# Optimization experiments

Measured on AMD Instinct MI355X. Metric: run time of the kernel, lower is better.

## Reference

```python
import jax, jax.numpy as jnp
import numpy as np

DIM = 1024
HEADS = 16
DIM_HEAD = 64
B = 4
N = 2048
INNER = HEADS * DIM_HEAD
SCALE = DIM_HEAD ** -0.5
NEG = -1e9


def setup_inputs() -> dict:
    key = jax.random.key(0)
    k1, k2, k3 = jax.random.split(key, 3)
    x = jax.random.normal(k1, (B, N, DIM), dtype=jnp.float32)
    w_qkv = jax.random.normal(k2, (DIM, 3 * INNER), dtype=jnp.float32) * (DIM ** -0.5)
    w_out = jax.random.normal(k3, (INNER, DIM), dtype=jnp.float32) * (INNER ** -0.5)
    b_out = jnp.zeros((DIM,), dtype=jnp.float32)
    return {"x": x, "w_qkv": w_qkv, "w_out": w_out, "b_out": b_out}


def reference(x, w_qkv, w_out, b_out):
    b, n, _ = x.shape
    qkv = x @ w_qkv  # [b, n, 3*inner]
    q, k, v = jnp.split(qkv, 3, axis=-1)
    # [b, n, inner] -> [b, h, n, d]
    split_heads = lambda t: t.reshape(b, n, HEADS, DIM_HEAD).transpose(0, 2, 1, 3)
    q, k, v = split_heads(q), split_heads(k), split_heads(v)
    dots = jnp.einsum('bhid,bhjd->bhij', q, k) * SCALE
    causal = jnp.tril(jnp.ones((n, n), dtype=bool))  # mask[i,j]=1 for j<=i
    dots = jnp.where(causal, dots, NEG)
    attn = jax.nn.softmax(dots, axis=-1)
    out = jnp.einsum('bhij,bhjd->bhid', attn, v)
    out = out.transpose(0, 2, 1, 3).reshape(b, n, INNER)
    return out @ w_out + b_out
```

## Files before the change

kernel.cpp:

```cpp
#include <hip/hip_runtime.h>

typedef unsigned short u16;
typedef unsigned int u32;
typedef __attribute__((ext_vector_type(8))) short short8;
typedef __attribute__((ext_vector_type(4))) float f32x4;
typedef __attribute__((ext_vector_type(4))) short short4v;
typedef __attribute__((ext_vector_type(2))) unsigned int uint2v;

#define MFMA_BF16(a, b, c) __builtin_amdgcn_mfma_f32_16x16x32_bf16((a), (b), (c), 0, 0, 0)

__device__ __forceinline__ void gl2lds16(const u16* g, u16* l) {
  __builtin_amdgcn_global_load_lds(
      (const __attribute__((address_space(1))) unsigned int*)g,
      (__attribute__((address_space(3))) unsigned int*)l, 16, 0, 0);
}

__device__ __forceinline__ u16 f2bf(float f) {
  union { float f; unsigned u; } v; v.f = f;
  unsigned r = v.u + 0x7fffu + ((v.u >> 16) & 1u);
  return (u16)(r >> 16);
}

__global__ void fill_one_f32(float* p, int n) {
  int i = blockIdx.x * blockDim.x + threadIdx.x;
  if (i < n) p[i] = 1.0f;
}

__global__ void prep_k(const float* __restrict__ x, u16* __restrict__ Xb,
                       const float* __restrict__ w_qkv, u16* __restrict__ wqkvT,
                       const float* __restrict__ w_out, u16* __restrict__ woutT) {
  __shared__ float tile[32][33];
  const int bid = blockIdx.x, t = threadIdx.x;
  if (bid < 2048) {
    const int base = (bid * 256 + t) * 16;
#pragma unroll
    for (int h = 0; h < 2; ++h) {
      const f32x4 v0 = *(const f32x4*)&x[base + h * 8];
      const f32x4 v1 = *(const f32x4*)&x[base + h * 8 + 4];
      short8 o;
      o[0] = (short)f2bf(v0.x); o[1] = (short)f2bf(v0.y);
      o[2] = (short)f2bf(v0.z); o[3] = (short)f2bf(v0.w);
      o[4] = (short)f2bf(v1.x); o[5] = (short)f2bf(v1.y);
      o[6] = (short)f2bf(v1.z); o[7] = (short)f2bf(v1.w);
      *(short8*)&Xb[base + h * 8] = o;
    }
    return;
  }
  const float* src; u16* dst; int R, C, bx, by;
  if (bid < 5120) {
    const int tb = bid - 2048;
    src = w_qkv; dst = wqkvT; R = 1024; C = 3072; bx = tb % 96; by = tb / 96;
  } else {
    const int tb = bid - 5120;
    src = w_out; dst = woutT; R = 1024; C = 1024; bx = tb % 32; by = tb / 32;
  }
  const int tx = t & 31, ty = t >> 5;
  const int r0 = by * 32, c0 = bx * 32;
#pragma unroll
  for (int i = 0; i < 4; ++i)
    tile[ty + i * 8][tx] = src[(size_t)(r0 + ty + i * 8) * C + c0 + tx];
  __syncthreads();
#pragma unroll
  for (int i = 0; i < 4; ++i)
    dst[(size_t)(c0 + ty + i * 8) * R + r0 + tx] = f2bf(tile[tx][ty + i * 8]);
}

template <int MODE>
__launch_bounds__(256, 2)
__global__ void gemm_bt_k(const u16* __restrict__ A, const u16* __restrict__ Bt,
                          int K, int Ncols,
                          u16* __restrict__ O0, u16* __restrict__ O1,
                          u16* __restrict__ O2,
                          float* __restrict__ Of, const float* __restrict__ biasf) {
  __shared__ __align__(16) u16 Alds[128 * 32];
  __shared__ __align__(16) u16 Blds[128 * 32];
  const int t = threadIdx.x;
  const int w = t >> 6, l = t & 63;
  const int quad = l >> 4, l16 = l & 15;
  const int m0 = blockIdx.y * 128, n0 = blockIdx.x * 128;
  const int wm = w & 1, wn = w >> 1;

  f32x4 acc[4][4];
#pragma unroll
  for (int a = 0; a < 4; ++a)
#pragma unroll
    for (int b = 0; b < 4; ++b) acc[a][b] = (f32x4){0.f, 0.f, 0.f, 0.f};

  const int c0 = w * 128 + l;

#pragma unroll 1
  for (int k0 = 0; k0 < K; k0 += 32) {
    {
      int c = c0;
      gl2lds16(A + (size_t)(m0 + (c >> 2)) * K + k0 + (c & 3) * 8,
               (u16*)((char*)Alds + c * 16));
      gl2lds16(Bt + (size_t)(n0 + (c >> 2)) * K + k0 + (c & 3) * 8,
               (u16*)((char*)Blds + c * 16));
      c = c0 + 64;
      gl2lds16(A + (size_t)(m0 + (c >> 2)) * K + k0 + (c & 3) * 8,
               (u16*)((char*)Alds + c * 16));
      gl2lds16(Bt + (size_t)(n0 + (c >> 2)) * K + k0 + (c & 3) * 8,
               (u16*)((char*)Blds + c * 16));
    }
    __syncthreads();
    short8 av[4], bv[4];
#pragma unroll
    for (int a = 0; a < 4; ++a)
      av[a] = *(const short8*)&Alds[(wm * 64 + a * 16 + l16) * 32 + quad * 8];
#pragma unroll
    for (int b = 0; b < 4; ++b)
      bv[b] = *(const short8*)&Blds[(wn * 64 + b * 16 + l16) * 32 + quad * 8];
#pragma unroll
    for (int a = 0; a < 4; ++a)
#pragma unroll
      for (int b = 0; b < 4; ++b)
        acc[a][b] = MFMA_BF16(av[a], bv[b], acc[a][b]);
    __syncthreads();
  }

#pragma unroll
  for (int a = 0; a < 4; ++a)
#pragma unroll
    for (int b = 0; b < 4; ++b) {
      const int row0 = m0 + wm * 64 + a * 16 + quad * 4;
      const int col = n0 + wn * 64 + b * 16 + l16;
      if (MODE == 0) {
        const int bb = row0 >> 11, n = row0 & 2047;
        const int which = col >> 10, j = col & 1023, h = j >> 6, d = j & 63;
        if (which == 2) {
          short4v o;
#pragma unroll
          for (int r = 0; r < 4; ++r) o[r] = (short)f2bf(acc[a][b][r]);
          *(short4v*)&O2[(((size_t)bb * 16 + h) * 64 + d) * 2048 + n] = o;
        } else {
          u16* dst = which ? O1 : O0;
#pragma unroll
          for (int r = 0; r < 4; ++r)
            dst[(((size_t)bb * 16 + h) * 2048 + (n + r)) * 64 + d] =
                f2bf(acc[a][b][r]);
        }
      } else {
#pragma unroll
        for (int r = 0; r < 4; ++r)
          Of[(size_t)(row0 + r) * Ncols + col] = acc[a][b][r] + biasf[col];
      }
    }
}

#define KSV 72
#define PS 72
__launch_bounds__(512, 2)
__global__ void flash_k8(const u16* __restrict__ Q, const u16* __restrict__ K,
                         const u16* __restrict__ VT, u16* __restrict__ AO) {
  __shared__ __align__(16) u16 Klds[2][64 * KSV];
  __shared__ __align__(16) u16 Vt[2][64 * KSV];
  __shared__ __align__(16) u16 Plds[8][16 * PS];
  const int t = threadIdx.x, w = t >> 6, l = t & 63;
  const int quad = l >> 4, l16 = l & 15;
  const int flat = blockIdx.x;
  const int bh = flat & 63;
  const int grp = flat >> 6;
  const int qi = (grp < 4) ? grp : (11 - grp);
  const size_t base = (size_t)bh * 2048 * 64;
  const u16* Qp = Q + base;
  const u16* Kp = K + base;
  const u16* VTp = VT + base;
  const int bb = bh >> 4, hh = bh & 15;
  const float SC = 0.125f;
  const float FM = 3.0f;

  const int kcp = t >> 3, kcd = (t & 7) * 8;
  const int vcd = t >> 3, vcp = (t & 7) * 8;

  short8 ones;
#pragma unroll
  for (int j = 0; j < 8; ++j) ones[j] = (short)0x3F80;

  const int qbase = qi * 256;

  short8 qf[2][2];
#pragma unroll
  for (int mi = 0; mi < 2; ++mi) {
    const int qrow = qbase + w * 32 + mi * 16 + l16;
    qf[mi][0] = *(const short8*)&Qp[(size_t)qrow * 64 + quad * 8];
    qf[mi][1] = *(const short8*)&Qp[(size_t)qrow * 64 + 32 + quad * 8];
  }

  f32x4 oacc[2][4], lacc[2];
#pragma unroll
  for (int mi = 0; mi < 2; ++mi) {
    lacc[mi] = (f32x4){0.f, 0.f, 0.f, 0.f};
#pragma unroll
    for (int df = 0; df < 4; ++df) oacc[mi][df] = (f32x4){0.f, 0.f, 0.f, 0.f};
  }

  const int nkt = 4 * qi + 4;
  const int wlo = qbase + w * 32;
  const int whi = wlo + 31;

  short8 kv = *(const short8*)&Kp[(size_t)kcp * 64 + kcd];
  short8 vv = *(const short8*)&VTp[(size_t)vcd * 2048 + vcp];

#pragma unroll 1
  for (int kt = 0; kt < nkt; ++kt) {
    const int buf = kt & 1;
    *(short8*)&Klds[buf][kcp * KSV + kcd] = kv;
    *(short8*)&Vt[buf][vcd * KSV + vcp] = vv;
    __syncthreads();

    if (kt + 1 < nkt) {
      kv = *(const short8*)&Kp[(size_t)((kt + 1) * 64 + kcp) * 64 + kcd];
      vv = *(const short8*)&VTp[(size_t)vcd * 2048 + (kt + 1) * 64 + vcp];
    }

    const bool skip = (kt * 64 > whi);
    if (!skip) {
      f32x4 sa[2][4];
#pragma unroll
      for (int nf = 0; nf < 4; ++nf) {
        const short8 kf0 = *(const short8*)&Klds[buf][(nf * 16 + l16) * KSV + quad * 8];
        const short8 kf1 = *(const short8*)&Klds[buf][(nf * 16 + l16) * KSV + 32 + quad * 8];
#pragma unroll
        for (int mi = 0; mi < 2; ++mi) {
          f32x4 s = (f32x4){0.f, 0.f, 0.f, 0.f};
          s = MFMA_BF16(kf0, qf[mi][0], s);
          s = MFMA_BF16(kf1, qf[mi][1], s);
          sa[mi][nf] = s;
        }
      }

      const bool needmask = (kt * 64 + 63 > wlo);
      short8 pf[2][2];
#pragma unroll
      for (int mi = 0; mi < 2; ++mi) {
        const int qrow = qbase + w * 32 + mi * 16 + l16;
#pragma unroll
        for (int nf = 0; nf < 4; ++nf) {
          u32 dw[2];
#pragma unroll
          for (int h = 0; h < 2; ++h) {
            u32 pk = 0;
#pragma unroll
            for (int r2 = 0; r2 < 2; ++r2) {
              const int r = h * 2 + r2;
              float arg = fmaf(sa[mi][nf][r], SC, -FM);
              if (needmask) {
                const int kp = kt * 64 + nf * 16 + quad * 4 + r;
                arg = (kp <= qrow) ? arg : -1e9f;
              }
              union { float f; unsigned u; } pu;
              pu.f = __expf(arg);
              pk |= (u32)((pu.u + 0x8000u) >> 16) << (16 * r2);
            }
            dw[h] = pk;
          }
          *(uint2v*)&Plds[w][l16 * PS + nf * 16 + quad * 4] = (uint2v){dw[0], dw[1]};
        }
        pf[mi][0] = *(const short8*)&Plds[w][l16 * PS + quad * 8];
        pf[mi][1] = *(const short8*)&Plds[w][l16 * PS + 32 + quad * 8];
        lacc[mi] = MFMA_BF16(pf[mi][0], ones, lacc[mi]);
        lacc[mi] = MFMA_BF16(pf[mi][1], ones, lacc[mi]);
      }

#pragma unroll
      for (int df = 0; df < 4; ++df) {
        const int rowb = (df * 16 + l16) * KSV;
        const short8 vf0 = *(const short8*)&Vt[buf][rowb + quad * 8];
        const short8 vf1 = *(const short8*)&Vt[buf][rowb + 32 + quad * 8];
#pragma unroll
        for (int mi = 0; mi < 2; ++mi) {
          oacc[mi][df] = MFMA_BF16(pf[mi][0], vf0, oacc[mi][df]);
          oacc[mi][df] = MFMA_BF16(pf[mi][1], vf1, oacc[mi][df]);
        }
      }
    }
  }

#pragma unroll
  for (int mi = 0; mi < 2; ++mi) {
    const int srow = qbase + w * 32 + mi * 16 + quad * 4;
#pragma unroll
    for (int df = 0; df < 4; ++df)
#pragma unroll
      for (int r = 0; r < 4; ++r) {
        const int n = srow + r;
        const int d = df * 16 + l16;
        AO[((size_t)bb * 2048 + n) * 1024 + hh * 64 + d] =
            f2bf(oacc[mi][df][r] / lacc[mi][r]);
      }
  }
}

extern "C" void kernel_launch(void* const* d_in, const int* in_sizes, int n_in,
                              void* d_out, int out_size, void* d_ws, size_t ws_size,
                              hipStream_t stream) {
  const float* x = (const float*)d_in[0];
  const float* w_qkv = (const float*)d_in[1];
  const float* w_out = (const float*)d_in[2];
  const float* b_out = (const float*)d_in[3];
  float* out = (float*)d_out;

  const size_t MB = 1024 * 1024;
  if (ws_size < 72 * MB) {
    fill_one_f32<<<(out_size + 255) / 256, 256, 0, stream>>>(out, out_size);
    return;
  }

  char* ws = (char*)d_ws;
  u16* wqkvT = (u16*)(ws);
  u16* woutT = (u16*)(ws + 6 * MB);
  u16* Xb = (u16*)(ws + 8 * MB);
  u16* AO = Xb;
  u16* Qb = (u16*)(ws + 24 * MB);
  u16* Kb = (u16*)(ws + 40 * MB);
  u16* VbT = (u16*)(ws + 56 * MB);

  prep_k<<<6144, 256, 0, stream>>>(x, Xb, w_qkv, wqkvT, w_out, woutT);
  gemm_bt_k<0><<<dim3(3072 / 128, 8192 / 128), 256, 0, stream>>>(
      Xb, wqkvT, 1024, 3072, Qb, Kb, VbT, nullptr, nullptr);
  flash_k8<<<512, 512, 0, stream>>>(Qb, Kb, VbT, AO);
  gemm_bt_k<1><<<dim3(1024 / 128, 8192 / 128), 256, 0, stream>>>(
      AO, woutT, 1024, 1024, nullptr, nullptr, nullptr, out, b_out);
}
```

Measured before the change: 254.5 us.

## Triple-buffer GEMM LDS loads with swizzle and 128x256 tiles

Reworks the bf16 GEMM kernel used for the QKV and output projections. LDS tiles are now triple-buffered so global-to-LDS loads for future k-steps run while MFMAs consume the current one, with vmcnt waits and raw barriers in place of full syncthreads. An XOR swizzle on LDS addresses is meant to cut bank conflicts. The block grows to 512 threads covering a 128x256 tile, and setprio is raised around the MFMA burst. The cost is more LDS per block, which may lower occupancy, and more hand-ordered synchronization.

New measurement: 287.5 us. 1.13x slower.

```diff
diff --git a/kernel.cpp b/kernel.cpp
--- a/kernel.cpp
+++ b/kernel.cpp
@@ -20,6 +20,8 @@
   unsigned r = v.u + 0x7fffu + ((v.u >> 16) & 1u);
   return (u16)(r >> 16);
 }
+
+__device__ __forceinline__ u32 swz(u32 x) { return x ^ (((x >> 7) & 7u) << 4); }
 
 __global__ void fill_one_f32(float* p, int n) {
   int i = blockIdx.x * blockDim.x + threadIdx.x;
@@ -65,20 +67,22 @@
     dst[(size_t)(c0 + ty + i * 8) * R + r0 + tx] = f2bf(tile[tx][ty + i * 8]);
 }
 
+#define ASLOT 8192
+#define BSLOT 16384
 template <int MODE>
-__launch_bounds__(256, 2)
+__launch_bounds__(512, 2)
 __global__ void gemm_bt_k(const u16* __restrict__ A, const u16* __restrict__ Bt,
                           int K, int Ncols,
                           u16* __restrict__ O0, u16* __restrict__ O1,
                           u16* __restrict__ O2,
                           float* __restrict__ Of, const float* __restrict__ biasf) {
-  __shared__ __align__(16) u16 Alds[128 * 32];
-  __shared__ __align__(16) u16 Blds[128 * 32];
+  __shared__ __align__(16) u16 Al[3 * ASLOT / 2];
+  __shared__ __align__(16) u16 Bl[3 * BSLOT / 2];
   const int t = threadIdx.x;
   const int w = t >> 6, l = t & 63;
   const int quad = l >> 4, l16 = l & 15;
-  const int m0 = blockIdx.y * 128, n0 = blockIdx.x * 128;
-  const int wm = w & 1, wn = w >> 1;
+  const int m0 = blockIdx.y * 128, n0 = blockIdx.x * 256;
+  const int wm = w >> 2, wn = w & 3;
 
   f32x4 acc[4][4];
 #pragma unroll
@@ -86,36 +90,102 @@
 #pragma unroll
     for (int b = 0; b < 4; ++b) acc[a][b] = (f32x4){0.f, 0.f, 0.f, 0.f};
 
-  const int c0 = w * 128 + l;
-
+  const u32 oA = (u32)t * 16u;
+  const u32 lA = swz(oA);
+  const u16* srcA = A + (size_t)(m0 + (lA >> 6)) * K + ((lA >> 4) & 3) * 8;
+  const u32 oB0 = (u32)t * 16u, oB1 = 8192u + (u32)t * 16u;
+  const u32 lB0 = swz(oB0), lB1 = swz(oB1);
+  const u16* srcB0 = Bt + (size_t)(n0 + (lB0 >> 6)) * K + ((lB0 >> 4) & 3) * 8;
+  const u16* srcB1 = Bt + (size_t)(n0 + (lB1 >> 6)) * K + ((lB1 >> 4) & 3) * 8;
+
+  u32 sa[4], sb[4];
+#pragma unroll
+  for (int a = 0; a < 4; ++a) {
+    const u32 row = wm * 64 + a * 16 + l16;
+    sa[a] = swz(row * 64 + quad * 16);
+  }
+#pragma unroll
+  for (int b = 0; b < 4; ++b) {
+    const u32 row = wn * 64 + b * 16 + l16;
+    sb[b] = swz(row * 64 + quad * 16);
+  }
+
+  const int NT = K >> 5;
+
+  gl2lds16(srcA, (u16*)((char*)Al + oA));
+  gl2lds16(srcB0, (u16*)((char*)Bl + oB0));
+  gl2lds16(srcB1, (u16*)((char*)Bl + oB1));
+  gl2lds16(srcA + 32, (u16*)((char*)Al + ASLOT + oA));
+  gl2lds16(srcB0 + 32, (u16*)((char*)Bl + BSLOT + oB0));
+  gl2lds16(srcB1 + 32, (u16*)((char*)Bl + BSLOT + oB1));
+  asm volatile("s_waitcnt vmcnt(3)" ::: "memory");
+  __builtin_amdgcn_s_barrier();
+
+  int rd = 0, st = 2;
+  int kel = 64;
 #pragma unroll 1
-  for (int k0 = 0; k0 < K; k0 += 32) {
+  for (int tt = 0; tt < NT - 2; ++tt) {
     {
-      int c = c0;
-      gl2lds16(A + (size_t)(m0 + (c >> 2)) * K + k0 + (c & 3) * 8,
-               (u16*)((char*)Alds + c * 16));
-      gl2lds16(Bt + (size_t)(n0 + (c >> 2)) * K + k0 + (c & 3) * 8,
-               (u16*)((char*)Blds + c * 16));
-      c = c0 + 64;
-      gl2lds16(A + (size_t)(m0 + (c >> 2)) * K + k0 + (c & 3) * 8,
-               (u16*)((char*)Alds + c * 16));
-      gl2lds16(Bt + (size_t)(n0 + (c >> 2)) * K + k0 + (c & 3) * 8,
-               (u16*)((char*)Blds + c * 16));
-    }
-    __syncthreads();
+      const u32 aoff = (u32)st * ASLOT, boff = (u32)st * BSLOT;
+      gl2lds16(srcA + kel, (u16*)((char*)Al + aoff + oA));
+      gl2lds16(srcB0 + kel, (u16*)((char*)Bl + boff + oB0));
+      gl2lds16(srcB1 + kel, (u16*)((char*)Bl + boff + oB1));
+      kel += 32;
+    }
+    const u32 ca = (u32)rd * ASLOT, cb = (u32)rd * BSLOT;
     short8 av[4], bv[4];
 #pragma unroll
     for (int a = 0; a < 4; ++a)
-      av[a] = *(const short8*)&Alds[(wm * 64 + a * 16 + l16) * 32 + quad * 8];
+      av[a] = *(const short8*)((const char*)Al + ca + sa[a]);
 #pragma unroll
     for (int b = 0; b < 4; ++b)
-      bv[b] = *(const short8*)&Blds[(wn * 64 + b * 16 + l16) * 32 + quad * 8];
+      bv[b] = *(const short8*)((const char*)Bl + cb + sb[b]);
+    asm volatile("s_waitcnt vmcnt(3)" ::: "memory");
+    __builtin_amdgcn_s_barrier();
+    __builtin_amdgcn_s_setprio(1);
 #pragma unroll
     for (int a = 0; a < 4; ++a)
 #pragma unroll
       for (int b = 0; b < 4; ++b)
         acc[a][b] = MFMA_BF16(av[a], bv[b], acc[a][b]);
-    __syncthreads();
+    __builtin_amdgcn_s_setprio(0);
+    __builtin_amdgcn_s_barrier();
+    rd = (rd == 2) ? 0 : rd + 1;
+    st = (st == 2) ? 0 : st + 1;
+  }
+  {
+    const u32 ca = (u32)rd * ASLOT, cb = (u32)rd * BSLOT;
+    short8 av[4], bv[4];
+#pragma unroll
+    for (int a = 0; a < 4; ++a)
+      av[a] = *(const short8*)((const char*)Al + ca + sa[a]);
+#pragma unroll
+    for (int b = 0; b < 4; ++b)
+      bv[b] = *(const short8*)((const char*)Bl + cb + sb[b]);
+    asm volatile("s_waitcnt vmcnt(0)" ::: "memory");
+    __builtin_amdgcn_s_barrier();
+#pragma unroll
+    for (int a = 0; a < 4; ++a)
+#pragma unroll
+      for (int b = 0; b < 4; ++b)
+        acc[a][b] = MFMA_BF16(av[a], bv[b], acc[a][b]);
+    __builtin_amdgcn_s_barrier();
+    rd = (rd == 2) ? 0 : rd + 1;
+  }
+  {
+    const u32 ca = (u32)rd * ASLOT, cb = (u32)rd * BSLOT;
+    short8 av[4], bv[4];
+#pragma unroll
+    for (int a = 0; a < 4; ++a)
+      av[a] = *(const short8*)((const char*)Al + ca + sa[a]);
+#pragma unroll
+    for (int b = 0; b < 4; ++b)
+      bv[b] = *(const short8*)((const char*)Bl + cb + sb[b]);
+#pragma unroll
+    for (int a = 0; a < 4; ++a)
+#pragma unroll
+      for (int b = 0; b < 4; ++b)
+        acc[a][b] = MFMA_BF16(av[a], bv[b], acc[a][b]);
   }
 
 #pragma unroll
@@ -316,9 +386,9 @@
   u16* VbT = (u16*)(ws + 56 * MB);
 
   prep_k<<<6144, 256, 0, stream>>>(x, Xb, w_qkv, wqkvT, w_out, woutT);
-  gemm_bt_k<0><<<dim3(3072 / 128, 8192 / 128), 256, 0, stream>>>(
+  gemm_bt_k<0><<<dim3(3072 / 256, 8192 / 128), 512, 0, stream>>>(
       Xb, wqkvT, 1024, 3072, Qb, Kb, VbT, nullptr, nullptr);
   flash_k8<<<512, 512, 0, stream>>>(Qb, Kb, VbT, AO);
-  gemm_bt_k<1><<<dim3(1024 / 128, 8192 / 128), 256, 0, stream>>>(
+  gemm_bt_k<1><<<dim3(1024 / 256, 8192 / 128), 512, 0, stream>>>(
       AO, woutT, 1024, 1024, nullptr, nullptr, nullptr, out, b_out);
 }
```

## Replace QKV GEMM with 256x256-tile double-buffered swizzled pipelined kernel

Applied to the files above, without the earlier changes.

Replaces the generic 128x128 QKV projection GEMM with a dedicated 512-thread kernel using 256x256 output tiles and K steps of 64. LDS is double-buffered and XOR-swizzled, filled through global_load_lds, and each K step is split into four quarter-phases that overlap the next loads with MFMA work, using manual barriers, vmcnt waits and setprio. The aim is more data reuse per tile, hidden global-load latency and fewer LDS bank conflicts. In exchange it needs 128KB of LDS per block, which limits occupancy, and the 384-block grid may leave a partial last wave.

After: 267.8 us. 5.2% more time.

```diff
diff --git a/kernel.cpp b/kernel.cpp
--- a/kernel.cpp
+++ b/kernel.cpp
@@ -20,6 +20,10 @@
   unsigned r = v.u + 0x7fffu + ((v.u >> 16) & 1u);
   return (u16)(r >> 16);
 }
+
+__device__ __forceinline__ void cfence() { asm volatile("" ::: "memory"); }
+
+__device__ __forceinline__ u32 swz(u32 x) { return x ^ (((x >> 7) & 7u) << 4); }
 
 __global__ void fill_one_f32(float* p, int n) {
   int i = blockIdx.x * blockDim.x + threadIdx.x;
@@ -65,13 +69,160 @@
     dst[(size_t)(c0 + ty + i * 8) * R + r0 + tx] = f2bf(tile[tx][ty + i * 8]);
 }
 
-template <int MODE>
+template <int AH, int BH, int WAIT, class S>
+__device__ __forceinline__ void qkv_phase(const u16* Al, const u16* Bl, int d,
+                                          const u32 (&aoff)[4][2],
+                                          const u32 (&boff)[2][2],
+                                          f32x4 (&acc)[2][2][4][2], S&& stage) {
+  const char* Ab = (const char*)Al + d * 32768 + AH * 16384;
+  const char* Bb = (const char*)Bl + d * 32768 + BH * 16384;
+  short8 af[4][2], bf[2][2];
+#pragma unroll
+  for (int mf = 0; mf < 4; ++mf)
+#pragma unroll
+    for (int ks = 0; ks < 2; ++ks)
+      af[mf][ks] = *(const short8*)(Ab + aoff[mf][ks]);
+#pragma unroll
+  for (int nf = 0; nf < 2; ++nf)
+#pragma unroll
+    for (int ks = 0; ks < 2; ++ks)
+      bf[nf][ks] = *(const short8*)(Bb + boff[nf][ks]);
+  stage();
+  cfence(); __builtin_amdgcn_s_barrier(); cfence();
+  __builtin_amdgcn_s_setprio(1);
+#pragma unroll
+  for (int mf = 0; mf < 4; ++mf)
+#pragma unroll
+    for (int nf = 0; nf < 2; ++nf)
+#pragma unroll
+      for (int ks = 0; ks < 2; ++ks)
+        acc[AH][BH][mf][nf] = MFMA_BF16(af[mf][ks], bf[nf][ks], acc[AH][BH][mf][nf]);
+  __builtin_amdgcn_s_setprio(0);
+  if (WAIT == 4) asm volatile("s_waitcnt vmcnt(4)" ::: "memory");
+  if (WAIT == 0) asm volatile("s_waitcnt vmcnt(0)" ::: "memory");
+  cfence(); __builtin_amdgcn_s_barrier(); cfence();
+}
+
+__launch_bounds__(512, 2)
+__global__ void gemm_qkv8p(const u16* __restrict__ A, const u16* __restrict__ Bt,
+                           int K, u16* __restrict__ O0, u16* __restrict__ O1,
+                           u16* __restrict__ O2) {
+  __shared__ __align__(16) u16 Al[32768];
+  __shared__ __align__(16) u16 Bl[32768];
+  const int t = threadIdx.x;
+  const int w = t >> 6, l = t & 63;
+  const int quad = l >> 4, l16 = l & 15;
+  const int m0 = blockIdx.y * 256, n0 = blockIdx.x * 256;
+  const int wm = w >> 2, wn = w & 3;
+
+  f32x4 acc[2][2][4][2];
+#pragma unroll
+  for (int ah = 0; ah < 2; ++ah)
+#pragma unroll
+    for (int bh = 0; bh < 2; ++bh)
+#pragma unroll
+      for (int mf = 0; mf < 4; ++mf)
+#pragma unroll
+        for (int nf = 0; nf < 2; ++nf)
+          acc[ah][bh][mf][nf] = (f32x4){0.f, 0.f, 0.f, 0.f};
+
+  const u32 oL = (u32)t * 16u;
+  const u32 lL = swz(oL);
+  const u32 grow = lL >> 7, gchunk = (lL >> 4) & 7u;
+  const u16* pAlo = A + (size_t)(m0 + grow) * K + gchunk * 8;
+  const u16* pBlo = Bt + (size_t)(n0 + grow) * K + gchunk * 8;
+
+#define STAGE_A(h_, kt_, d_)                                        \
+  do {                                                              \
+    char* _dst = (char*)Al + (d_) * 32768 + (h_) * 16384;           \
+    const u16* _s = pAlo + (size_t)(h_) * 128 * K + (size_t)(kt_) * 64; \
+    gl2lds16(_s, (u16*)(_dst + oL));                                \
+    gl2lds16(_s + (size_t)64 * K, (u16*)(_dst + oL + 8192));        \
+  } while (0)
+#define STAGE_B(h_, kt_, d_)                                        \
+  do {                                                              \
+    char* _dst = (char*)Bl + (d_) * 32768 + (h_) * 16384;           \
+    const u16* _s = pBlo + (size_t)(h_) * 128 * K + (size_t)(kt_) * 64; \
+    gl2lds16(_s, (u16*)(_dst + oL));                                \
+    gl2lds16(_s + (size_t)64 * K, (u16*)(_dst + oL + 8192));        \
+  } while (0)
+
+  u32 aoff[4][2], boff[2][2];
+#pragma unroll
+  for (int mf = 0; mf < 4; ++mf)
+#pragma unroll
+    for (int ks = 0; ks < 2; ++ks)
+      aoff[mf][ks] = swz((u32)((wm * 64 + mf * 16 + l16) * 128 + ks * 64 + quad * 16));
+#pragma unroll
+  for (int nf = 0; nf < 2; ++nf)
+#pragma unroll
+    for (int ks = 0; ks < 2; ++ks)
+      boff[nf][ks] = swz((u32)((wn * 32 + nf * 16 + l16) * 128 + ks * 64 + quad * 16));
+
+  const int NT = K >> 6;
+
+  STAGE_A(0, 0, 0); STAGE_A(1, 0, 0); STAGE_B(0, 0, 0); STAGE_B(1, 0, 0);
+  STAGE_B(0, 1, 1); STAGE_A(1, 1, 1);
+  asm volatile("s_waitcnt vmcnt(4)" ::: "memory");
+  cfence(); __builtin_amdgcn_s_barrier(); cfence();
+
+#pragma unroll 1
+  for (int j = 0; j < NT - 2; ++j) {
+    const int d = j & 1, dn = d ^ 1;
+    qkv_phase<0, 0, -1>(Al, Bl, d, aoff, boff, acc, [&] { STAGE_B(1, j + 1, dn); });
+    qkv_phase<1, 0, -1>(Al, Bl, d, aoff, boff, acc, [&] { STAGE_A(0, j + 1, dn); });
+    qkv_phase<1, 1, -1>(Al, Bl, d, aoff, boff, acc, [&] { STAGE_B(0, j + 2, d); });
+    qkv_phase<0, 1, 4>(Al, Bl, d, aoff, boff, acc, [&] { STAGE_A(1, j + 2, d); });
+  }
+  {
+    const int j = NT - 2, d = j & 1, dn = d ^ 1;
+    qkv_phase<0, 0, -1>(Al, Bl, d, aoff, boff, acc, [&] { STAGE_B(1, j + 1, dn); });
+    qkv_phase<1, 0, -1>(Al, Bl, d, aoff, boff, acc, [&] { STAGE_A(0, j + 1, dn); });
+    qkv_phase<1, 1, -1>(Al, Bl, d, aoff, boff, acc, [&] {});
+    qkv_phase<0, 1, 0>(Al, Bl, d, aoff, boff, acc, [&] {});
+  }
+  {
+    const int d = (NT - 1) & 1;
+    qkv_phase<0, 0, -1>(Al, Bl, d, aoff, boff, acc, [&] {});
+    qkv_phase<1, 0, -1>(Al, Bl, d, aoff, boff, acc, [&] {});
+    qkv_phase<1, 1, -1>(Al, Bl, d, aoff, boff, acc, [&] {});
+    qkv_phase<0, 1, -1>(Al, Bl, d, aoff, boff, acc, [&] {});
+  }
+#undef STAGE_A
+#undef STAGE_B
+
+#pragma unroll
+  for (int ah = 0; ah < 2; ++ah)
+#pragma unroll
+    for (int bh = 0; bh < 2; ++bh)
+#pragma unroll
+      for (int mf = 0; mf < 4; ++mf)
+#pragma unroll
+        for (int nf = 0; nf < 2; ++nf) {
+          const int row0 = m0 + ah * 128 + wm * 64 + mf * 16 + quad * 4;
+          const int col = n0 + bh * 128 + wn * 32 + nf * 16 + l16;
+          const int bb = row0 >> 11, n = row0 & 2047;
+          const int which = col >> 10, jj = col & 1023, h = jj >> 6, dd = jj & 63;
+          const f32x4 v = acc[ah][bh][mf][nf];
+          if (which == 2) {
+            short4v o;
+#pragma unroll
+            for (int r = 0; r < 4; ++r) o[r] = (short)f2bf(v[r]);
+            *(short4v*)&O2[(((size_t)bb * 16 + h) * 64 + dd) * 2048 + n] = o;
+          } else {
+            u16* dst = which ? O1 : O0;
+#pragma unroll
+            for (int r = 0; r < 4; ++r)
+              dst[(((size_t)bb * 16 + h) * 2048 + (n + r)) * 64 + dd] =
+                  f2bf(v[r]);
+          }
+        }
+}
+
 __launch_bounds__(256, 2)
-__global__ void gemm_bt_k(const u16* __restrict__ A, const u16* __restrict__ Bt,
-                          int K, int Ncols,
-                          u16* __restrict__ O0, u16* __restrict__ O1,
-                          u16* __restrict__ O2,
-                          float* __restrict__ Of, const float* __restrict__ biasf) {
+__global__ void gemm_out_k(const u16* __restrict__ A, const u16* __restrict__ Bt,
+                           int K, int Ncols,
+                           float* __restrict__ Of, const float* __restrict__ biasf) {
   __shared__ __align__(16) u16 Alds[128 * 32];
   __shared__ __align__(16) u16 Blds[128 * 32];
   const int t = threadIdx.x;
@@ -124,26 +275,9 @@
     for (int b = 0; b < 4; ++b) {
       const int row0 = m0 + wm * 64 + a * 16 + quad * 4;
       const int col = n0 + wn * 64 + b * 16 + l16;
-      if (MODE == 0) {
-        const int bb = row0 >> 11, n = row0 & 2047;
-        const int which = col >> 10, j = col & 1023, h = j >> 6, d = j & 63;
-        if (which == 2) {
-          short4v o;
-#pragma unroll
-          for (int r = 0; r < 4; ++r) o[r] = (short)f2bf(acc[a][b][r]);
-          *(short4v*)&O2[(((size_t)bb * 16 + h) * 64 + d) * 2048 + n] = o;
-        } else {
-          u16* dst = which ? O1 : O0;
-#pragma unroll
-          for (int r = 0; r < 4; ++r)
-            dst[(((size_t)bb * 16 + h) * 2048 + (n + r)) * 64 + d] =
-                f2bf(acc[a][b][r]);
-        }
-      } else {
-#pragma unroll
-        for (int r = 0; r < 4; ++r)
-          Of[(size_t)(row0 + r) * Ncols + col] = acc[a][b][r] + biasf[col];
-      }
+#pragma unroll
+      for (int r = 0; r < 4; ++r)
+        Of[(size_t)(row0 + r) * Ncols + col] = acc[a][b][r] + biasf[col];
     }
 }
 
@@ -316,9 +450,9 @@
   u16* VbT = (u16*)(ws + 56 * MB);
 
   prep_k<<<6144, 256, 0, stream>>>(x, Xb, w_qkv, wqkvT, w_out, woutT);
-  gemm_bt_k<0><<<dim3(3072 / 128, 8192 / 128), 256, 0, stream>>>(
-      Xb, wqkvT, 1024, 3072, Qb, Kb, VbT, nullptr, nullptr);
+  gemm_qkv8p<<<dim3(3072 / 256, 8192 / 256), 512, 0, stream>>>(
+      Xb, wqkvT, 1024, Qb, Kb, VbT);
   flash_k8<<<512, 512, 0, stream>>>(Qb, Kb, VbT, AO);
-  gemm_bt_k<1><<<dim3(1024 / 128, 8192 / 128), 256, 0, stream>>>(
-      AO, woutT, 1024, 1024, nullptr, nullptr, nullptr, out, b_out);
-}
+  gemm_out_k<<<dim3(1024 / 128, 8192 / 128), 256, 0, stream>>>(
+      AO, woutT, 1024, 1024, out, b_out);
+}
```
